# Kernel optimization log

Hardware: AMD Instinct MI355X
Metric: run time of the kernel (lower is better)

Reference implementation:

```python
import jax, jax.numpy as jnp
import numpy as np

D_MODEL = 512
N_HEAD = 8
D_K = 64
D_V = 64
D_HID = 2048
N_LAYERS = 2
BATCH = 16384
SEQ = 8
N_AGENTS = 8  # agent_index = i % 8 in original Encoder.forward
LN_EPS = 1e-6


def sinusoid_table(n_pos, d):
    # matches PositionalEncoding._get_sinusoid_encoding_table
    pos = jnp.arange(n_pos, dtype=jnp.float32)[:, None]              # [P,1]
    j = jnp.arange(d, dtype=jnp.float32)[None, :]                     # [1,D]
    angle = pos / jnp.power(10000.0, 2.0 * jnp.floor(j / 2.0) / d)    # [P,D]
    even = jnp.sin(angle[:, 0::2])
    odd = jnp.cos(angle[:, 1::2])
    tab = jnp.zeros((n_pos, d), jnp.float32)
    tab = tab.at[:, 0::2].set(even).at[:, 1::2].set(odd)
    return tab


def layer_norm(x, g, b):
    mu = jnp.mean(x, axis=-1, keepdims=True)
    var = jnp.mean(jnp.square(x - mu), axis=-1, keepdims=True)
    return (x - mu) * jax.lax.rsqrt(var + LN_EPS) * g + b


def setup_inputs() -> dict:
    key = jax.random.key(0)
    ks = jax.random.split(key, 8)
    s_attn = 1.0 / np.sqrt(D_MODEL)
    s_ffn1 = 1.0 / np.sqrt(D_MODEL)
    s_ffn2 = 1.0 / np.sqrt(D_HID)
    L = N_LAYERS
    return {
        "x": jax.random.normal(ks[0], (BATCH, SEQ, D_MODEL), jnp.float32),
        "Wq": jax.random.normal(ks[1], (L, D_MODEL, N_HEAD * D_K), jnp.float32) * s_attn,
        "bq": jnp.zeros((L, N_HEAD * D_K), jnp.float32),
        "Wk": jax.random.normal(ks[2], (L, D_MODEL, N_HEAD * D_K), jnp.float32) * s_attn,
        "bk": jnp.zeros((L, N_HEAD * D_K), jnp.float32),
        "Wv": jax.random.normal(ks[3], (L, D_MODEL, N_HEAD * D_V), jnp.float32) * s_attn,
        "bv": jnp.zeros((L, N_HEAD * D_V), jnp.float32),
        "Wo": jax.random.normal(ks[4], (L, N_HEAD * D_V, D_MODEL), jnp.float32) * s_attn,
        "bo": jnp.zeros((L, D_MODEL), jnp.float32),
        "ln1_g": jnp.ones((L, D_MODEL), jnp.float32),
        "ln1_b": jnp.zeros((L, D_MODEL), jnp.float32),
        "W1": jax.random.normal(ks[5], (L, D_MODEL, D_HID), jnp.float32) * s_ffn1,
        "b1": jnp.zeros((L, D_HID), jnp.float32),
        "W2": jax.random.normal(ks[6], (L, D_HID, D_MODEL), jnp.float32) * s_ffn2,
        "b2": jnp.zeros((L, D_MODEL), jnp.float32),
        "ln2_g": jnp.ones((L, D_MODEL), jnp.float32),
        "ln2_b": jnp.zeros((L, D_MODEL), jnp.float32),
    }


def reference(x, Wq, bq, Wk, bk, Wv, bv, Wo, bo, ln1_g, ln1_b,
              W1, b1, W2, b2, ln2_g, ln2_b):
    B, S, D = x.shape
    # positional encoding add (PositionalEncoding.forward)
    h = x + sinusoid_table(S, D)[None, :, :]
    scale = 1.0 / np.sqrt(D_K)
    for l in range(N_LAYERS):
        # --- multi-head self attention (post-LN residual) ---
        q = (h @ Wq[l] + bq[l]).reshape(B, S, N_HEAD, D_K)
        k = (h @ Wk[l] + bk[l]).reshape(B, S, N_HEAD, D_K)
        v = (h @ Wv[l] + bv[l]).reshape(B, S, N_HEAD, D_V)
        scores = jnp.einsum("bqhd,bkhd->bhqk", q, k) * scale
        attn = jax.nn.softmax(scores, axis=-1)
        ctx = jnp.einsum("bhqk,bkhd->bqhd", attn, v).reshape(B, S, N_HEAD * D_V)
        h = layer_norm(ctx @ Wo[l] + bo[l] + h, ln1_g[l], ln1_b[l])
        # --- position-wise FFN (post-LN residual) ---
        ffn = jax.nn.relu(h @ W1[l] + b1[l]) @ W2[l] + b2[l]
        h = layer_norm(ffn + h, ln2_g[l], ln2_b[l])
    # enc_out[i] = enc_input[i % 8]  (vectorized agent-token gather)
    idx = jnp.arange(B) % N_AGENTS
    return h[jnp.arange(B), idx]  # [B, D_MODEL]
```

## Files before the change

### kernel.cpp

```cpp
#include <hip/hip_runtime.h>

typedef unsigned short u16;
typedef unsigned int u32;
typedef __attribute__((ext_vector_type(8))) unsigned short u16x8;
typedef __attribute__((ext_vector_type(4))) float f32x4;

#define NTOK 131072
#define NSEL 16384

__device__ __forceinline__ float b2f(u16 v) {
  return __uint_as_float(((u32)v) << 16);
}
__device__ __forceinline__ u16 f2b(float f) {
  u32 u = __float_as_uint(f);
  u32 r = u + 0x7fffu + ((u >> 16) & 1u);
  return (u16)(r >> 16);
}

__device__ __forceinline__ void gload16(const void* g, void* l) {
  __builtin_amdgcn_global_load_lds((const __attribute__((address_space(1))) void*)g,
                                   (__attribute__((address_space(3))) void*)l, 16, 0, 0);
}

__device__ __forceinline__ void mfma16(f32x4& c, u16x8 a, u16x8 b) {
  asm("v_mfma_f32_16x16x32_bf16 %0, %1, %2, %0" : "+v"(c) : "v"(a), "v"(b));
}

#define BAR() __builtin_amdgcn_s_barrier()
#define VM(n) asm volatile("s_waitcnt vmcnt(" #n ")" ::: "memory")
#define PRIO1() __builtin_amdgcn_s_setprio(1)
#define PRIO0() __builtin_amdgcn_s_setprio(0)

__global__ __launch_bounds__(256) void table_kernel(float* __restrict__ tab) {
  const int i = blockIdx.x * 256 + threadIdx.x;
  if (i >= 4096) return;
  const int p = i >> 9, j = i & 511;
  const float ex = 2.f * (float)(j >> 1) / 512.f;
  const float ang = (float)p * powf(10000.f, -ex);
  tab[i] = (j & 1) ? cosf(ang) : sinf(ang);
}

__global__ __launch_bounds__(256) void biaspack_kernel(const float* __restrict__ bq,
                                                       const float* __restrict__ bk,
                                                       const float* __restrict__ bv,
                                                       float* __restrict__ dst) {
  const int i = blockIdx.x * 256 + threadIdx.x;
  if (i >= 3072) return;
  const int l = i / 1536, j = i % 1536;
  float v;
  if (j < 512) v = bq[l * 512 + j];
  else if (j < 1024) v = bk[l * 512 + j - 512];
  else v = bv[l * 512 + j - 1024];
  dst[i] = v;
}

struct TJob { const float* src; u16* dst; int Ki, Ni, blk0; };
struct TJobs { TJob j[12]; };

__global__ __launch_bounds__(256) void wconv_kernel(TJobs jobs) {
  __shared__ float tile[64][65];
  const int bid = blockIdx.x;
  int ji = 0;
#pragma unroll
  for (int t = 1; t < 12; ++t)
    if (bid >= jobs.j[t].blk0) ji = t;
  const TJob J = jobs.j[ji];
  const int rel = bid - J.blk0;
  const int ntn = J.Ni >> 6;
  const int tk = rel / ntn, tn = rel % ntn;
  const int tid = threadIdx.x;
  const int cn = tid & 63, rk = tid >> 6;
#pragma unroll
  for (int r = 0; r < 16; ++r) {
    const int kk = rk + r * 4;
    tile[kk][cn] = J.src[(size_t)(tk * 64 + kk) * J.Ni + tn * 64 + cn];
  }
  __syncthreads();
  const int ck = tid & 63, rn = tid >> 6;
#pragma unroll
  for (int r = 0; r < 16; ++r) {
    const int nn = rn + r * 4;
    J.dst[(size_t)(tn * 64 + nn) * J.Ki + tk * 64 + ck] = f2b(tile[ck][nn]);
  }
}

__global__ __launch_bounds__(256) void posenc_kernel(const float* __restrict__ x,
                                                     const float* __restrict__ tab,
                                                     u16* __restrict__ h) {
  const int i = blockIdx.x * 256 + threadIdx.x;
  const size_t e0 = (size_t)i * 8;
  const int d = (int)(e0 & 511);
  const int srow = (int)((e0 >> 9) & 7);
  const float4 a0 = *(const float4*)(x + e0);
  const float4 a1 = *(const float4*)(x + e0 + 4);
  const float* tp = tab + srow * 512 + d;
  float v[8] = {a0.x, a0.y, a0.z, a0.w, a1.x, a1.y, a1.z, a1.w};
  u16x8 o;
#pragma unroll
  for (int e = 0; e < 8; ++e) o[e] = f2b(v[e] + tp[e]);
  *(u16x8*)(h + e0) = o;
}

#define RDA(c, mh)                                                                  \
  A0 = *(const u16x8*)&As[c][wrbase + ((((mh) << 6) + 0 + lr) << 6) + swk0];        \
  A1 = *(const u16x8*)&As[c][wrbase + ((((mh) << 6) + 0 + lr) << 6) + swk1];        \
  A2 = *(const u16x8*)&As[c][wrbase + ((((mh) << 6) + 16 + lr) << 6) + swk0];       \
  A3 = *(const u16x8*)&As[c][wrbase + ((((mh) << 6) + 16 + lr) << 6) + swk1];       \
  A4 = *(const u16x8*)&As[c][wrbase + ((((mh) << 6) + 32 + lr) << 6) + swk0];       \
  A5 = *(const u16x8*)&As[c][wrbase + ((((mh) << 6) + 32 + lr) << 6) + swk1];       \
  A6 = *(const u16x8*)&As[c][wrbase + ((((mh) << 6) + 48 + lr) << 6) + swk0];       \
  A7 = *(const u16x8*)&As[c][wrbase + ((((mh) << 6) + 48 + lr) << 6) + swk1]

#define RDB(c, nh, V00, V01, V10, V11)                                                   \
  V00 = *(const u16x8*)&Bs[c][wcbase + ((brow0 + (((nh) << 1) + 0) * 16 + lr) << 6) + swk0]; \
  V01 = *(const u16x8*)&Bs[c][wcbase + ((brow0 + (((nh) << 1) + 0) * 16 + lr) << 6) + swk1]; \
  V10 = *(const u16x8*)&Bs[c][wcbase + ((brow0 + (((nh) << 1) + 1) * 16 + lr) << 6) + swk0]; \
  V11 = *(const u16x8*)&Bs[c][wcbase + ((brow0 + (((nh) << 1) + 1) * 16 + lr) << 6) + swk1]

#define QM(mh, nh, V00, V01, V10, V11)                \
  mfma16(acc[((mh) << 2) + 0][((nh) << 1) + 0], A0, V00); \
  mfma16(acc[((mh) << 2) + 0][((nh) << 1) + 1], A0, V10); \
  mfma16(acc[((mh) << 2) + 1][((nh) << 1) + 0], A2, V00); \
  mfma16(acc[((mh) << 2) + 1][((nh) << 1) + 1], A2, V10); \
  mfma16(acc[((mh) << 2) + 2][((nh) << 1) + 0], A4, V00); \
  mfma16(acc[((mh) << 2) + 2][((nh) << 1) + 1], A4, V10); \
  mfma16(acc[((mh) << 2) + 3][((nh) << 1) + 0], A6, V00); \
  mfma16(acc[((mh) << 2) + 3][((nh) << 1) + 1], A6, V10); \
  mfma16(acc[((mh) << 2) + 0][((nh) << 1) + 0], A1, V01); \
  mfma16(acc[((mh) << 2) + 0][((nh) << 1) + 1], A1, V11); \
  mfma16(acc[((mh) << 2) + 1][((nh) << 1) + 0], A3, V01); \
  mfma16(acc[((mh) << 2) + 1][((nh) << 1) + 1], A3, V11); \
  mfma16(acc[((mh) << 2) + 2][((nh) << 1) + 0], A5, V01); \
  mfma16(acc[((mh) << 2) + 2][((nh) << 1) + 1], A5, V11); \
  mfma16(acc[((mh) << 2) + 3][((nh) << 1) + 0], A7, V01); \
  mfma16(acc[((mh) << 2) + 3][((nh) << 1) + 1], A7, V11)

template <int RELU>
__global__ __launch_bounds__(512, 1) void gemm256(const u16* __restrict__ A,
                                                  const u16* __restrict__ Bt,
                                                  const float* __restrict__ bias,
                                                  u16* __restrict__ C, int M, int N, int K) {
  __shared__ __align__(16) u16 As[2][16384];
  __shared__ __align__(16) u16 Bs[2][16384];
  const int nbn = N >> 8;
  const int cpx = gridDim.x >> 3;
  const int bid = blockIdx.x;
  const int wgid = (bid & 7) * cpx + (bid >> 3);
  const int bm = wgid / nbn, bn = wgid - bm * nbn;
  const int tid = threadIdx.x;
  const int wid = tid >> 6, lane = tid & 63;
  const int wr = wid >> 2, wc = wid & 3;
  const int lr = lane & 15, kg0 = lane >> 4;
  const int swk0 = ((kg0 ^ (lr & 7)) << 3);
  const int swk1 = (((kg0 + 4) ^ (lr & 7)) << 3);
  const int wrbase = wr << 13;
  const int wcbase = (wc >> 1) << 13;
  const int brow0 = (wc & 1) << 6;
  const int rowinc = tid >> 3;
  const int gcol = (((tid & 7) ^ (rowinc & 7)) << 3);
  const u16* Ag = A + (size_t)((bm << 8) + rowinc) * K + gcol;
  const u16* Bg = Bt + (size_t)((bn << 8) + rowinc) * K + gcol;
  const int ldsw = wid << 9;

  f32x4 acc[8][4];
  const f32x4 zero = {0.f, 0.f, 0.f, 0.f};
#pragma unroll
  for (int m = 0; m < 8; ++m)
#pragma unroll
    for (int n = 0; n < 4; ++n) acc[m][n] = zero;

  u16x8 A0, A1, A2, A3, A4, A5, A6, A7;
  u16x8 B00, B01, B10, B11;
  u16x8 C00, C01, C10, C11;

  auto stgA = [&](int c, int h, int koff) {
    gload16(Ag + (size_t)(h << 7) * K + koff, &As[c][(h << 13) + ldsw]);
    gload16(Ag + (size_t)((h << 7) + 64) * K + koff, &As[c][(h << 13) + 4096 + ldsw]);
  };
  auto stgB = [&](int c, int h, int koff) {
    gload16(Bg + (size_t)(h << 7) * K + koff, &Bs[c][(h << 13) + ldsw]);
    gload16(Bg + (size_t)((h << 7) + 64) * K + koff, &Bs[c][(h << 13) + 4096 + ldsw]);
  };

  stgA(0, 0, 0); stgA(0, 1, 0); stgB(0, 0, 0); stgB(0, 1, 0);
  stgB(1, 0, 64); stgB(1, 1, 64);
  VM(4);
  BAR();

  const int niter = K >> 7;
  int k1 = 64, k2 = 128, k3 = 192;
#pragma unroll 1
  for (int i = 0; i < niter - 1; ++i) {
    RDA(0, 0); RDB(0, 0, B00, B01, B10, B11); stgA(1, 0, k1);
    PRIO1(); QM(0, 0, B00, B01, B10, B11); PRIO0();
    RDB(0, 1, C00, C01, C10, C11); stgA(1, 1, k1);
    PRIO1(); QM(0, 1, C00, C01, C10, C11); PRIO0(); BAR();
    RDA(0, 1); stgB(0, 0, k2);
    PRIO1(); QM(1, 1, C00, C01, C10, C11); PRIO0();
    stgB(0, 1, k2);
    PRIO1(); QM(1, 0, B00, B01, B10, B11); PRIO0(); VM(4); BAR();
    RDA(1, 0); RDB(1, 0, B00, B01, B10, B11); stgA(0, 0, k2);
    PRIO1(); QM(0, 0, B00, B01, B10, B11); PRIO0();
    RDB(1, 1, C00, C01, C10, C11); stgA(0, 1, k2);
    PRIO1(); QM(0, 1, C00, C01, C10, C11); PRIO0(); BAR();
    RDA(1, 1); stgB(1, 0, k3);
    PRIO1(); QM(1, 1, C00, C01, C10, C11); PRIO0();
    stgB(1, 1, k3);
    PRIO1(); QM(1, 0, B00, B01, B10, B11); PRIO0(); VM(4); BAR();
    k1 += 128; k2 += 128; k3 += 128;
  }
  RDA(0, 0); RDB(0, 0, B00, B01, B10, B11); stgA(1, 0, k1);
  PRIO1(); QM(0, 0, B00, B01, B10, B11); PRIO0();
  RDB(0, 1, C00, C01, C10, C11); stgA(1, 1, k1);
  PRIO1(); QM(0, 1, C00, C01, C10, C11); PRIO0(); BAR();
  RDA(0, 1);
  PRIO1(); QM(1, 1, C00, C01, C10, C11); PRIO0();
  PRIO1(); QM(1, 0, B00, B01, B10, B11); PRIO0(); VM(0); BAR();
  RDA(1, 0); RDB(1, 0, B00, B01, B10, B11);
  PRIO1(); QM(0, 0, B00, B01, B10, B11); PRIO0();
  RDB(1, 1, C00, C01, C10, C11);
  PRIO1(); QM(0, 1, C00, C01, C10, C11); PRIO0(); BAR();
  RDA(1, 1);
  PRIO1(); QM(1, 1, C00, C01, C10, C11); PRIO0();
  PRIO1(); QM(1, 0, B00, B01, B10, B11); PRIO0();

  const int r0 = kg0 << 2;
  const int cc = lr;
#pragma unroll
  for (int m8 = 0; m8 < 8; ++m8) {
    const size_t grow = (size_t)((bm << 8) + (wr << 7) + (m8 << 4) + r0);
#pragma unroll
    for (int n4 = 0; n4 < 4; ++n4) {
      const int gc = (bn << 8) + (wc << 6) + (n4 << 4) + cc;
      const float bv = bias[gc];
#pragma unroll
      for (int rr = 0; rr < 4; ++rr) {
        float v = acc[m8][n4][rr] + bv;
        if (RELU) v = fmaxf(v, 0.f);
        C[(grow + rr) * (size_t)N + gc] = f2b(v);
      }
    }
  }
}

template <int SEL>
__global__ __launch_bounds__(256) void attn_kernel(const u16* __restrict__ QKV,
                                                   u16* __restrict__ ctx) {
  __shared__ __align__(16) u16 sm[4][3][8][72];
  __shared__ float at[4][8][8];
  const int tid = threadIdx.x;
  const int wid = tid >> 6, lane = tid & 63;
  const int bh = blockIdx.x * 4 + wid;
  const int b = bh >> 3, h = bh & 7;
  const int s = lane >> 3, g = lane & 7;
  const u16* base = QKV + (size_t)(b * 8 + s) * 1536 + h * 64 + g * 8;
#pragma unroll
  for (int t = 0; t < 3; ++t)
    *(u16x8*)&sm[wid][t][s][g * 8] = *(const u16x8*)(base + t * 512);
  __syncthreads();
  float sc = 0.f;
#pragma unroll
  for (int c = 0; c < 8; ++c) {
    const int cg = ((c + g) & 7) * 8;
    u16x8 qv = *(const u16x8*)&sm[wid][0][s][cg];
    u16x8 kv = *(const u16x8*)&sm[wid][1][g][cg];
#pragma unroll
    for (int e = 0; e < 8; ++e) sc += b2f(qv[e]) * b2f(kv[e]);
  }
  sc *= 0.125f;
  float mx = fmaxf(sc, __shfl_xor(sc, 1));
  mx = fmaxf(mx, __shfl_xor(mx, 2));
  mx = fmaxf(mx, __shfl_xor(mx, 4));
  const float ex = __expf(sc - mx);
  float sum = ex;
  sum += __shfl_xor(sum, 1);
  sum += __shfl_xor(sum, 2);
  sum += __shfl_xor(sum, 4);
  at[wid][s][g] = ex / sum;
  __syncthreads();
  float o[8] = {0.f, 0.f, 0.f, 0.f, 0.f, 0.f, 0.f, 0.f};
#pragma unroll
  for (int j = 0; j < 8; ++j) {
    const float a = at[wid][s][j];
    u16x8 vv = *(const u16x8*)&sm[wid][2][j][g * 8];
#pragma unroll
    for (int e = 0; e < 8; ++e) o[e] += a * b2f(vv[e]);
  }
  u16x8 ov;
#pragma unroll
  for (int e = 0; e < 8; ++e) ov[e] = f2b(o[e]);
  if (SEL) {
    if (s == (b & 7))
      *(u16x8*)(ctx + (size_t)b * 512 + h * 64 + g * 8) = ov;
  } else {
    *(u16x8*)(ctx + (size_t)(b * 8 + s) * 512 + h * 64 + g * 8) = ov;
  }
}

__global__ __launch_bounds__(256) void ln_kernel(const u16* __restrict__ t,
                                                 u16* __restrict__ h,
                                                 const float* __restrict__ gam,
                                                 const float* __restrict__ bet) {
  const int tid = threadIdx.x;
  const int wid = tid >> 6, lane = tid & 63;
  const int row = blockIdx.x * 4 + wid;
  const size_t base = (size_t)row * 512 + lane * 8;
  u16x8 tv = *(const u16x8*)(t + base);
  u16x8 hv = *(const u16x8*)(h + base);
  float x[8];
  float s1 = 0.f, s2 = 0.f;
#pragma unroll
  for (int e = 0; e < 8; ++e) {
    x[e] = b2f(tv[e]) + b2f(hv[e]);
    s1 += x[e];
    s2 += x[e] * x[e];
  }
#pragma unroll
  for (int m = 1; m < 64; m <<= 1) {
    s1 += __shfl_xor(s1, m);
    s2 += __shfl_xor(s2, m);
  }
  const float mu = s1 * (1.f / 512.f);
  const float var = s2 * (1.f / 512.f) - mu * mu;
  const float rs = rsqrtf(var + 1e-6f);
  const float4 g0 = *(const float4*)(gam + lane * 8);
  const float4 g1 = *(const float4*)(gam + lane * 8 + 4);
  const float4 b0 = *(const float4*)(bet + lane * 8);
  const float4 b1 = *(const float4*)(bet + lane * 8 + 4);
  const float gv[8] = {g0.x, g0.y, g0.z, g0.w, g1.x, g1.y, g1.z, g1.w};
  const float bv[8] = {b0.x, b0.y, b0.z, b0.w, b1.x, b1.y, b1.z, b1.w};
  u16x8 yv;
#pragma unroll
  for (int e = 0; e < 8; ++e) yv[e] = f2b((x[e] - mu) * rs * gv[e] + bv[e]);
  *(u16x8*)(h + base) = yv;
}

__global__ __launch_bounds__(256) void ln_gather_kernel(const u16* __restrict__ t,
                                                        const u16* __restrict__ h,
                                                        u16* __restrict__ hsel,
                                                        const float* __restrict__ gam,
                                                        const float* __restrict__ bet) {
  const int tid = threadIdx.x;
  const int wid = tid >> 6, lane = tid & 63;
  const int b = blockIdx.x * 4 + wid;
  const size_t tb = (size_t)(b * 8 + (b & 7));
  u16x8 tv = *(const u16x8*)(t + (size_t)b * 512 + lane * 8);
  u16x8 hv = *(const u16x8*)(h + tb * 512 + lane * 8);
  float x[8];
  float s1 = 0.f, s2 = 0.f;
#pragma unroll
  for (int e = 0; e < 8; ++e) {
    x[e] = b2f(tv[e]) + b2f(hv[e]);
    s1 += x[e];
    s2 += x[e] * x[e];
  }
#pragma unroll
  for (int m = 1; m < 64; m <<= 1) {
    s1 += __shfl_xor(s1, m);
    s2 += __shfl_xor(s2, m);
  }
  const float mu = s1 * (1.f / 512.f);
  const float var = s2 * (1.f / 512.f) - mu * mu;
  const float rs = rsqrtf(var + 1e-6f);
  const float4 g0 = *(const float4*)(gam + lane * 8);
  const float4 g1 = *(const float4*)(gam + lane * 8 + 4);
  const float4 b0 = *(const float4*)(bet + lane * 8);
  const float4 b1 = *(const float4*)(bet + lane * 8 + 4);
  const float gv[8] = {g0.x, g0.y, g0.z, g0.w, g1.x, g1.y, g1.z, g1.w};
  const float bv[8] = {b0.x, b0.y, b0.z, b0.w, b1.x, b1.y, b1.z, b1.w};
  u16x8 yv;
#pragma unroll
  for (int e = 0; e < 8; ++e) yv[e] = f2b((x[e] - mu) * rs * gv[e] + bv[e]);
  *(u16x8*)(hsel + (size_t)b * 512 + lane * 8) = yv;
}

__global__ __launch_bounds__(256) void ln_final_kernel(const u16* __restrict__ t,
                                                       const u16* __restrict__ hsel,
                                                       const float* __restrict__ gam,
                                                       const float* __restrict__ bet,
                                                       float* __restrict__ out) {
  const int tid = threadIdx.x;
  const int wid = tid >> 6, lane = tid & 63;
  const int b = blockIdx.x * 4 + wid;
  const size_t base = (size_t)b * 512 + lane * 8;
  u16x8 tv = *(const u16x8*)(t + base);
  u16x8 hv = *(const u16x8*)(hsel + base);
  float x[8];
  float s1 = 0.f, s2 = 0.f;
#pragma unroll
  for (int e = 0; e < 8; ++e) {
    x[e] = b2f(tv[e]) + b2f(hv[e]);
    s1 += x[e];
    s2 += x[e] * x[e];
  }
#pragma unroll
  for (int m = 1; m < 64; m <<= 1) {
    s1 += __shfl_xor(s1, m);
    s2 += __shfl_xor(s2, m);
  }
  const float mu = s1 * (1.f / 512.f);
  const float var = s2 * (1.f / 512.f) - mu * mu;
  const float rs = rsqrtf(var + 1e-6f);
  const float4 g0 = *(const float4*)(gam + lane * 8);
  const float4 g1 = *(const float4*)(gam + lane * 8 + 4);
  const float4 b0 = *(const float4*)(bet + lane * 8);
  const float4 b1 = *(const float4*)(bet + lane * 8 + 4);
  const float gv[8] = {g0.x, g0.y, g0.z, g0.w, g1.x, g1.y, g1.z, g1.w};
  const float bv[8] = {b0.x, b0.y, b0.z, b0.w, b1.x, b1.y, b1.z, b1.w};
  float y[8];
#pragma unroll
  for (int e = 0; e < 8; ++e) y[e] = (x[e] - mu) * rs * gv[e] + bv[e];
  float4* op = (float4*)(out + base);
  op[0] = make_float4(y[0], y[1], y[2], y[3]);
  op[1] = make_float4(y[4], y[5], y[6], y[7]);
}

static void launch_gemm(const u16* A, const u16* Bt, const float* bias, u16* C, int M, int N,
                        int K, int relu, hipStream_t st) {
  dim3 grid((M >> 8) * (N >> 8));
  if (relu)
    gemm256<1><<<grid, 512, 0, st>>>(A, Bt, bias, C, M, N, K);
  else
    gemm256<0><<<grid, 512, 0, st>>>(A, Bt, bias, C, M, N, K);
}

extern "C" void kernel_launch(void* const* d_in, const int* in_sizes, int n_in, void* d_out,
                              int out_size, void* d_ws, size_t ws_size, hipStream_t stream) {
  const float* x = (const float*)d_in[0];
  const float* Wq = (const float*)d_in[1];
  const float* bq = (const float*)d_in[2];
  const float* Wk = (const float*)d_in[3];
  const float* bk = (const float*)d_in[4];
  const float* Wv = (const float*)d_in[5];
  const float* bv = (const float*)d_in[6];
  const float* Wo = (const float*)d_in[7];
  const float* bo = (const float*)d_in[8];
  const float* ln1g = (const float*)d_in[9];
  const float* ln1b = (const float*)d_in[10];
  const float* W1 = (const float*)d_in[11];
  const float* b1 = (const float*)d_in[12];
  const float* W2 = (const float*)d_in[13];
  const float* b2 = (const float*)d_in[14];
  const float* ln2g = (const float*)d_in[15];
  const float* ln2b = (const float*)d_in[16];
  float* out = (float*)d_out;

  char* ws = (char*)d_ws;
  const size_t o_tab = 0;
  const size_t o_bqkv = 16384;
  const size_t o_w = 28672;
  const size_t o_h = o_w + 12582912;
  const size_t o_buf = o_h + (size_t)NTOK * 512 * 2;
  const size_t o_tmp = o_buf + (size_t)NTOK * 2048 * 2;
  const size_t o_hsel = o_tmp + (size_t)NTOK * 512 * 2;
  const size_t need = o_hsel + (size_t)NSEL * 512 * 2;
  if (ws_size < need) return;

  float* tab = (float*)(ws + o_tab);
  float* bqkv = (float*)(ws + o_bqkv);
  u16* wbf = (u16*)(ws + o_w);
  u16* h = (u16*)(ws + o_h);
  u16* buf = (u16*)(ws + o_buf);
  u16* ctx = buf + (size_t)NTOK * 1536;
  u16* tmp = (u16*)(ws + o_tmp);
  u16* hsel = (u16*)(ws + o_hsel);

  table_kernel<<<16, 256, 0, stream>>>(tab);
  biaspack_kernel<<<12, 256, 0, stream>>>(bq, bk, bv, bqkv);

  TJobs jobs;
  int blk = 0, nj = 0;
  auto add = [&](const float* s, u16* dmat, int Ki, int Ni) {
    jobs.j[nj].src = s;
    jobs.j[nj].dst = dmat;
    jobs.j[nj].Ki = Ki;
    jobs.j[nj].Ni = Ni;
    jobs.j[nj].blk0 = blk;
    ++nj;
    blk += (Ki / 64) * (Ni / 64);
  };
  for (int l = 0; l < 2; ++l) {
    u16* wl = wbf + (size_t)l * 3145728;
    add(Wq + (size_t)l * 262144, wl, 512, 512);
    add(Wk + (size_t)l * 262144, wl + 262144, 512, 512);
    add(Wv + (size_t)l * 262144, wl + 524288, 512, 512);
    add(Wo + (size_t)l * 262144, wl + 786432, 512, 512);
    add(W1 + (size_t)l * 1048576, wl + 1048576, 512, 2048);
    add(W2 + (size_t)l * 1048576, wl + 2097152, 2048, 512);
  }
  wconv_kernel<<<blk, 256, 0, stream>>>(jobs);
  posenc_kernel<<<32768, 256, 0, stream>>>(x, tab, h);

  {
    u16* wl = wbf;
    launch_gemm(h, wl, bqkv, buf, NTOK, 1536, 512, 0, stream);
    attn_kernel<0><<<32768, 256, 0, stream>>>(buf, ctx);
    launch_gemm(ctx, wl + 786432, bo, tmp, NTOK, 512, 512, 0, stream);
    ln_kernel<<<32768, 256, 0, stream>>>(tmp, h, ln1g, ln1b);
    launch_gemm(h, wl + 1048576, b1, buf, NTOK, 2048, 512, 1, stream);
    launch_gemm(buf, wl + 2097152, b2, tmp, NTOK, 512, 2048, 0, stream);
    ln_kernel<<<32768, 256, 0, stream>>>(tmp, h, ln2g, ln2b);
  }

  {
    u16* wl = wbf + 3145728;
    u16* ctx_sel = ctx;
    u16* tmp_sel = tmp;
    u16* hid_sel = buf;
    launch_gemm(h, wl, bqkv + 1536, buf, NTOK, 1536, 512, 0, stream);
    attn_kernel<1><<<32768, 256, 0, stream>>>(buf, ctx_sel);
    launch_gemm(ctx_sel, wl + 786432, bo + 512, tmp_sel, NSEL, 512, 512, 0, stream);
    ln_gather_kernel<<<NSEL / 4, 256, 0, stream>>>(tmp_sel, h, hsel, ln1g + 512, ln1b + 512);
    launch_gemm(hsel, wl + 1048576, b1 + 2048, hid_sel, NSEL, 2048, 512, 1, stream);
    launch_gemm(hid_sel, wl + 2097152, b2 + 512, tmp_sel, NSEL, 512, 2048, 0, stream);
    ln_final_kernel<<<NSEL / 4, 256, 0, stream>>>(tmp_sel, hsel, ln2g + 512, ln2b + 512, out);
  }
}
```

Measured before the change: 1.707 ms.

## Compute layer-2 queries only for selected tokens and fuse gather into LN

In the last layer only one query token per batch row is needed, so the Q projection is now computed only for the 16384 gathered rows while K and V are still projected for all tokens. The second layer-1 LayerNorm additionally writes the selected rows to a compact buffer, and a new attention kernel handles a single query per (batch, head). This removes about a third of the last-layer QKV GEMM work and cuts attention compute, at the cost of one extra small GEMM launch and a slightly more complex buffer layout.

After: 1.636 ms, median of 2. -4.1%, faster.

```diff
diff --git a/kernel.cpp b/kernel.cpp
--- a/kernel.cpp
+++ b/kernel.cpp
@@ -243,7 +243,6 @@
   }
 }
 
-template <int SEL>
 __global__ __launch_bounds__(256) void attn_kernel(const u16* __restrict__ QKV,
                                                    u16* __restrict__ ctx) {
   __shared__ __align__(16) u16 sm[4][3][8][72];
@@ -289,18 +288,66 @@
   u16x8 ov;
 #pragma unroll
   for (int e = 0; e < 8; ++e) ov[e] = f2b(o[e]);
-  if (SEL) {
-    if (s == (b & 7))
-      *(u16x8*)(ctx + (size_t)b * 512 + h * 64 + g * 8) = ov;
-  } else {
-    *(u16x8*)(ctx + (size_t)(b * 8 + s) * 512 + h * 64 + g * 8) = ov;
-  }
-}
-
+  *(u16x8*)(ctx + (size_t)(b * 8 + s) * 512 + h * 64 + g * 8) = ov;
+}
+
+__global__ __launch_bounds__(256) void attn_sel_kernel(const u16* __restrict__ KV,
+                                                       const u16* __restrict__ Qs,
+                                                       u16* __restrict__ ctx) {
+  __shared__ __align__(16) u16 sm[4][2][8][72];
+  __shared__ float at[4][8];
+  const int tid = threadIdx.x;
+  const int wid = tid >> 6, lane = tid & 63;
+  const int bh = blockIdx.x * 4 + wid;
+  const int b = bh >> 3, h = bh & 7;
+  const int s = lane >> 3, g = lane & 7;
+  const u16* base = KV + (size_t)(b * 8 + s) * 1024 + h * 64 + g * 8;
+  *(u16x8*)&sm[wid][0][s][g * 8] = *(const u16x8*)(base);
+  *(u16x8*)&sm[wid][1][s][g * 8] = *(const u16x8*)(base + 512);
+  const u16x8 qv = *(const u16x8*)(Qs + (size_t)b * 512 + h * 64 + g * 8);
+  __syncthreads();
+  float p = 0.f;
+  {
+    u16x8 kv8 = *(const u16x8*)&sm[wid][0][s][g * 8];
+#pragma unroll
+    for (int e = 0; e < 8; ++e) p += b2f(qv[e]) * b2f(kv8[e]);
+  }
+  p += __shfl_xor(p, 1);
+  p += __shfl_xor(p, 2);
+  p += __shfl_xor(p, 4);
+  p *= 0.125f;
+  float mx = fmaxf(p, __shfl_xor(p, 8));
+  mx = fmaxf(mx, __shfl_xor(mx, 16));
+  mx = fmaxf(mx, __shfl_xor(mx, 32));
+  const float ex = __expf(p - mx);
+  float sum = ex;
+  sum += __shfl_xor(sum, 8);
+  sum += __shfl_xor(sum, 16);
+  sum += __shfl_xor(sum, 32);
+  if (g == 0) at[wid][s] = ex / sum;
+  __syncthreads();
+  if (s == 0) {
+    float o[8] = {0.f, 0.f, 0.f, 0.f, 0.f, 0.f, 0.f, 0.f};
+#pragma unroll
+    for (int j = 0; j < 8; ++j) {
+      const float a = at[wid][j];
+      u16x8 vv = *(const u16x8*)&sm[wid][1][j][g * 8];
+#pragma unroll
+      for (int e = 0; e < 8; ++e) o[e] += a * b2f(vv[e]);
+    }
+    u16x8 ov;
+#pragma unroll
+    for (int e = 0; e < 8; ++e) ov[e] = f2b(o[e]);
+    *(u16x8*)(ctx + (size_t)b * 512 + h * 64 + g * 8) = ov;
+  }
+}
+
+template <int GATHER>
 __global__ __launch_bounds__(256) void ln_kernel(const u16* __restrict__ t,
                                                  u16* __restrict__ h,
                                                  const float* __restrict__ gam,
-                                                 const float* __restrict__ bet) {
+                                                 const float* __restrict__ bet,
+                                                 u16* __restrict__ hgat) {
   const int tid = threadIdx.x;
   const int wid = tid >> 6, lane = tid & 63;
   const int row = blockIdx.x * 4 + wid;
@@ -333,6 +380,11 @@
 #pragma unroll
   for (int e = 0; e < 8; ++e) yv[e] = f2b((x[e] - mu) * rs * gv[e] + bv[e]);
   *(u16x8*)(h + base) = yv;
+  if (GATHER) {
+    const int bb = row >> 3;
+    if ((row & 7) == (bb & 7))
+      *(u16x8*)(hgat + (size_t)bb * 512 + lane * 8) = yv;
+  }
 }
 
 __global__ __launch_bounds__(256) void ln_gather_kernel(const u16* __restrict__ t,
@@ -453,7 +505,8 @@
   const size_t o_buf = o_h + (size_t)NTOK * 512 * 2;
   const size_t o_tmp = o_buf + (size_t)NTOK * 2048 * 2;
   const size_t o_hsel = o_tmp + (size_t)NTOK * 512 * 2;
-  const size_t need = o_hsel + (size_t)NSEL * 512 * 2;
+  const size_t o_hgat = o_hsel + (size_t)NSEL * 512 * 2;
+  const size_t need = o_hgat + (size_t)NSEL * 512 * 2;
   if (ws_size < need) return;
 
   float* tab = (float*)(ws + o_tab);
@@ -464,6 +517,7 @@
   u16* ctx = buf + (size_t)NTOK * 1536;
   u16* tmp = (u16*)(ws + o_tmp);
   u16* hsel = (u16*)(ws + o_hsel);
+  u16* hgat = (u16*)(ws + o_hgat);
 
   table_kernel<<<16, 256, 0, stream>>>(tab);
   biaspack_kernel<<<12, 256, 0, stream>>>(bq, bk, bv, bqkv);
@@ -494,21 +548,24 @@
   {
     u16* wl = wbf;
     launch_gemm(h, wl, bqkv, buf, NTOK, 1536, 512, 0, stream);
-    attn_kernel<0><<<32768, 256, 0, stream>>>(buf, ctx);
+    attn_kernel<<<32768, 256, 0, stream>>>(buf, ctx);
     launch_gemm(ctx, wl + 786432, bo, tmp, NTOK, 512, 512, 0, stream);
-    ln_kernel<<<32768, 256, 0, stream>>>(tmp, h, ln1g, ln1b);
+    ln_kernel<0><<<32768, 256, 0, stream>>>(tmp, h, ln1g, ln1b, nullptr);
     launch_gemm(h, wl + 1048576, b1, buf, NTOK, 2048, 512, 1, stream);
     launch_gemm(buf, wl + 2097152, b2, tmp, NTOK, 512, 2048, 0, stream);
-    ln_kernel<<<32768, 256, 0, stream>>>(tmp, h, ln2g, ln2b);
+    ln_kernel<1><<<32768, 256, 0, stream>>>(tmp, h, ln2g, ln2b, hgat);
   }
 
   {
     u16* wl = wbf + 3145728;
-    u16* ctx_sel = ctx;
+    u16* kv = buf;
+    u16* qsel = buf + (size_t)NTOK * 1024;
+    u16* ctx_sel = qsel + (size_t)NSEL * 512;
+    u16* hid_sel = ctx_sel + (size_t)NSEL * 512;
     u16* tmp_sel = tmp;
-    u16* hid_sel = buf;
-    launch_gemm(h, wl, bqkv + 1536, buf, NTOK, 1536, 512, 0, stream);
-    attn_kernel<1><<<32768, 256, 0, stream>>>(buf, ctx_sel);
+    launch_gemm(h, wl + 262144, bqkv + 1536 + 512, kv, NTOK, 1024, 512, 0, stream);
+    launch_gemm(hgat, wl, bqkv + 1536, qsel, NSEL, 512, 512, 0, stream);
+    attn_sel_kernel<<<32768, 256, 0, stream>>>(kv, qsel, ctx_sel);
     launch_gemm(ctx_sel, wl + 786432, bo + 512, tmp_sel, NSEL, 512, 512, 0, stream);
     ln_gather_kernel<<<NSEL / 4, 256, 0, stream>>>(tmp_sel, h, hsel, ln1g + 512, ln1b + 512);
     launch_gemm(hsel, wl + 1048576, b1 + 2048, hid_sel, NSEL, 2048, 512, 1, stream);
```
